# Kernel tuning notes

Measured on AMD Instinct MI355X. Metric: run time of the kernel, lower is better.

Reference implementation:

```python
import jax, jax.numpy as jnp
import numpy as np

# ---- problem constants (match init_kwargs) ----
LAM = 1.0; MU = 1.0; D0 = 1.0; NMIN = 1.0; NMAX = 99; ALPHA = 2.0
BATCH = 2048; N_STEPS = 64; T = 1.0; HIDDEN = 128


def _U(x):
    return D0 / (x + NMIN) ** ALPHA


def _delta_n(pre_n, dt, forward, k, rng):
    # faithful numpy port of PolymerDiffusion.delta_N (jump sizes shared across batch per call)
    log_res = -np.log(rng.random(k))
    lsk = np.concatenate([[0.0], np.cumsum(log_res / LAM / 2)])
    msk = np.concatenate([[0.0], np.cumsum(log_res / MU / 2)])
    jl = int(np.searchsorted(lsk[1:], dt, side='right'))  # first j with dt < lsk[j+1]
    jm = int(np.searchsorted(msk[1:], dt, side='right'))
    if jl >= k: jl = 0  # no break -> delta stays 0
    if jm >= k: jm = 0
    eta = rng.random(pre_n.shape[0])
    if forward:
        d_up = np.where(pre_n <= NMAX - jl, jl, 0)
        d_dn = np.where(pre_n >= jm, -jm, 0)
    else:
        d_up = np.where(pre_n >= jl, jl, 0)
        d_dn = np.where(pre_n <= NMAX - jm, -jm, 0)
    return np.where(eta < 0.5, d_up, d_dn).astype(np.float64)


def _get_samples(dt, N, rng):
    B = BATCH
    X1 = np.zeros((B, N + 1)); X1[:, 0] = rng.integers(0, NMAX + 1, B)
    X2 = np.zeros((B, N + 1))
    dB = rng.standard_normal((B, N)) * np.sqrt(dt)
    for i in range(N):
        X1[:, i + 1] = X1[:, i] + _delta_n(X1[:, i], dt, True, 5, rng)
        X2[:, i + 1] = X2[:, i] + _U(X1[:, i]) * dt + dB[:, i]
    X1b = rng.integers(0, NMAX + 1, (B, N + 1)).astype(np.float64)
    X2b = np.zeros((B, N + 1))
    dBb = rng.standard_normal((B, N)) * np.sqrt(dt)
    X1b[:, N] = X1[:, N]; X2b[:, N] = X2[:, N]
    for i in range(N):
        X1b[:, N - i - 1] = X1b[:, N - i] - _delta_n(X1b[:, N - i], dt, False, 5, rng)
        X2b[:, N - i - 1] = X2b[:, N - i] - _U(X1b[:, N - i]) * dt - dBb[:, N - i - 1]
    return (np.concatenate([X1, X1b], 0), np.concatenate([X2, X2b], 0), np.concatenate([dB, dBb], 0))


def setup_inputs() -> dict:
    rng = np.random.default_rng(0)
    dt = T / N_STEPS
    n_np, s_np, dB_np = _get_samples(dt, N_STEPS, rng)
    key = jax.random.key(0)
    ks = jax.random.split(key, 4)
    def w(k, fi, fo):
        return jax.random.normal(k, (fi, fo), jnp.float32) / np.sqrt(fi).astype(np.float32)
    return {
        'W1': w(ks[0], 2, HIDDEN), 'b1': jnp.zeros(HIDDEN, jnp.float32),
        'W2': w(ks[1], HIDDEN, HIDDEN), 'b2': jnp.zeros(HIDDEN, jnp.float32),
        'W3': w(ks[2], HIDDEN, HIDDEN), 'b3': jnp.zeros(HIDDEN, jnp.float32),
        'W4': w(ks[3], HIDDEN, NMAX + 1), 'b4': jnp.zeros(NMAX + 1, jnp.float32),
        'samples_n': jnp.asarray(n_np, jnp.int32),      # [2B, N+1]
        'samples_s': jnp.asarray(s_np, jnp.float32),    # [2B, N+1]
        'samples_deltaB': jnp.asarray(dB_np, jnp.float32),  # [2B, N]
        't': jnp.float32(T),
    }


def reference(W1, b1, W2, b2, W3, b3, W4, b4, samples_n, samples_s, samples_deltaB, t):
    N = samples_deltaB.shape[1]
    dt = t / N
    out_dim = W4.shape[1]  # nmax + 1

    def u_scalar(s, tk, n):
        x = jnp.stack([s, tk])  # [2]
        h = jnp.tanh(x @ W1 + b1)
        h = jnp.tanh(h @ W2 + b2)
        h = jnp.tanh(h @ W3 + b3)
        return (h @ W4 + b4)[n]

    du = jax.grad(u_scalar, 0)
    ddu = jax.grad(du, 0)
    u_v = jax.vmap(u_scalar)
    du_v = jax.vmap(du)
    ddu_v = jax.vmap(ddu)

    B2 = samples_s.shape[0]
    tk0 = jnp.broadcast_to(t, (B2,))
    sN, nN = samples_s[:, N], samples_n[:, N]
    u = u_v(sN, tk0, nN)
    ps = du_v(sN, tk0, nN)
    pss = ddu_v(sN, tk0, nN)

    # step i uses column N-1-i and time tk = t - i*dt (tk decremented AFTER get_partial, as in source)
    dB_rev = samples_deltaB[:, ::-1].T            # [N, 2B]
    s_rev = samples_s[:, N - 1::-1].T             # [N, 2B]
    n_rev = samples_n[:, N - 1::-1].T             # [N, 2B]
    tks = t - dt * jnp.arange(N, dtype=samples_s.dtype)  # [N]

    def step(carry, xs):
        u, ps, pss = carry
        dB, s_col, n_col, tk = xs
        u = u - ps * dB - pss * dt * 0.5
        tkv = jnp.broadcast_to(tk, s_col.shape)
        ps = du_v(s_col, tkv, n_col)
        pss = ddu_v(s_col, tkv, n_col)
        return (u, ps, pss), None

    (u, _, _), _ = jax.lax.scan(step, (u, ps, pss), (dB_rev, s_rev, n_rev, tks))

    beta = 1e6
    s0 = samples_s[:, 0]
    u0 = jnp.sqrt(beta / (2 * jnp.pi)) * jnp.exp(-beta * s0 ** 2 / 2) / out_dim
    return (u[:, None], u0[:, None])
```

## Files before the change

kernel.cpp:

```cpp
#include <hip/hip_runtime.h>
#include <hip/hip_fp16.h>
#include <math.h>

#define HIDDEN 128
#define NSTEP  64
#define BATCH2 4096
#define OUTD   100

typedef __attribute__((ext_vector_type(4))) _Float16 f16x4;
typedef __attribute__((ext_vector_type(8))) _Float16 f16x8;
typedef __attribute__((ext_vector_type(4))) float    f32x4;

static __device__ __forceinline__ f32x4 mfma16(f16x4 a, f16x4 b, f32x4 c) {
    return __builtin_amdgcn_mfma_f32_16x16x16f16(a, b, c, 0, 0, 0);
}
static __device__ __forceinline__ unsigned h2u(__half2 h) {
    return __builtin_bit_cast(unsigned, h);
}
static __device__ __forceinline__ __half2 u2h(unsigned u) {
    return __builtin_bit_cast(__half2, u);
}
static __device__ __forceinline__ f16x4 frag2(__half2 lo, __half2 hi) {
    uint2 p = { h2u(lo), h2u(hi) };
    return __builtin_bit_cast(f16x4, p);
}

static __device__ __forceinline__ void load_lds16(const void* g, void* l) {
    __builtin_amdgcn_global_load_lds(
        (const __attribute__((address_space(1))) void*)g,
        (__attribute__((address_space(3))) void*)l, 16, 0, 0);
}

static __device__ __forceinline__ void tanh_chain_h2(
    __half2 z, __half2 zd, __half2 zdd,
    __half2& a, __half2& ad, __half2& add)
{
    const __half2 one = __float2half2_rn(1.0f);
    const __half2 two = __float2half2_rn(2.0f);
    __half2 e = h2exp(__hadd2(z, z));
    __half2 w = __hmul2(two, h2rcp(__hadd2(e, one)));
    a  = __hsub2(one, w);
    __half2 g = __hmul2(w, __hsub2(two, w));
    ad = __hmul2(g, zd);
    __half2 p = __hmul2(a, zd);
    __half2 u = __hadd2(p, p);
    add = __hsub2(__hmul2(g, zdd), __hmul2(u, ad));
}

__global__ __launch_bounds__(256) void setup_kernel(
    const float* __restrict__ W2, const float* __restrict__ W3,
    const float* __restrict__ W4,
    const float* __restrict__ samples_s,
    __half* __restrict__ wbf, float* __restrict__ out)
{
    int t = blockIdx.x * blockDim.x + threadIdx.x;
    int l   = t >> 14;
    int pos = t & 16383;
    int chunk = pos >> 9;
    int mt = chunk >> 2, kp = chunk & 3;
    int lane = (pos >> 3) & 63;
    int i = pos & 7;
    int row = 16 * mt + (lane & 15);
    int k   = 32 * kp + 16 * (i >> 2) + 4 * (lane >> 4) + (i & 3);
    const float* W = l ? W3 : W2;
    wbf[t] = __float2half(W[k * HIDDEN + row]);
    if (t < OUTD * HIDDEN) {
        int nn = t >> 7, h = t & 127;
        wbf[32768 + t] = __float2half(W4[h * OUTD + nn]);
    }
    if (t < BATCH2) {
        out[t] = 0.0f;
        float s0 = samples_s[t * (NSTEP + 1)];
        out[BATCH2 + t] = 3.9894228040143267f * expf(-500000.0f * s0 * s0);
    }
}

__global__ __launch_bounds__(256, 3) void eval_kernel(
    const float* __restrict__ W1, const float* __restrict__ b1,
    const float* __restrict__ b2, const float* __restrict__ b3,
    const float* __restrict__ b4,
    const __half* __restrict__ wbf,
    const int*   __restrict__ samples_n,
    const float* __restrict__ samples_s,
    const float* __restrict__ samples_dB,
    const float* __restrict__ tptr,
    float* __restrict__ out)
{
    __shared__ __align__(16) short ldsW[HIDDEN * HIDDEN];
    __shared__ float ldsB2[HIDDEN];
    __shared__ float ldsB3[HIDDEN];

    const int tid  = threadIdx.x;
    const int w    = tid >> 6;
    const int lane = tid & 63;
    const int m16  = lane & 15;
    const int q    = lane >> 4;
    const int b    = blockIdx.x;

    if (tid < HIDDEN) {
        ldsB2[tid] = b2[tid];
        ldsB3[tid] = b3[tid];
    }
    {
        const short* g2 = (const short*)wbf;
        #pragma unroll
        for (int it = 0; it < 8; ++it) {
            int idx = w * 8 + it;
            load_lds16(g2 + idx * 512 + lane * 8, ldsW + idx * 512);
        }
    }

    const float t  = tptr[0];
    const float dt = t / (float)NSTEP;
    const int   j  = 16 * w + m16;
    const int   c  = NSTEP - j;
    const float s  = samples_s[b * (NSTEP + 1) + c];
    const int   n  = samples_n[b * (NSTEP + 1) + c];
    const float dB = samples_dB[b * NSTEP + (NSTEP - 1 - j)];
    const float tk = (j == 0) ? t : t - dt * (float)(j - 1);

    f16x4 Bv[8], Bd[8], Bdd[8];
    const __half2 zero2 = __float2half2_rn(0.0f);
    #pragma unroll
    for (int kt = 0; kt < 8; ++kt) {
        const int h0 = 16 * kt + 4 * q;
        float4 wa = *(const float4*)(W1 + h0);
        float4 wb = *(const float4*)(W1 + HIDDEN + h0);
        float4 bb = *(const float4*)(b1 + h0);
        __half2 z0 = __floats2half2_rn(fmaf(wa.x, s, fmaf(wb.x, tk, bb.x)),
                                       fmaf(wa.y, s, fmaf(wb.y, tk, bb.y)));
        __half2 z1 = __floats2half2_rn(fmaf(wa.z, s, fmaf(wb.z, tk, bb.z)),
                                       fmaf(wa.w, s, fmaf(wb.w, tk, bb.w)));
        __half2 zd0 = __floats2half2_rn(wa.x, wa.y);
        __half2 zd1 = __floats2half2_rn(wa.z, wa.w);
        __half2 a0, ad0, add0, a1, ad1, add1;
        tanh_chain_h2(z0, zd0, zero2, a0, ad0, add0);
        tanh_chain_h2(z1, zd1, zero2, a1, ad1, add1);
        Bv[kt]  = frag2(a0,  a1);
        Bd[kt]  = frag2(ad0, ad1);
        Bdd[kt] = frag2(add0, add1);
    }

    __syncthreads();

    f16x4 Nv[8], Nd[8], Ndd[8];
    #pragma unroll
    for (int mt = 0; mt < 8; ++mt) {
        f32x4 aV = {0.f,0.f,0.f,0.f}, aD = {0.f,0.f,0.f,0.f}, aDD = {0.f,0.f,0.f,0.f};
        #pragma unroll
        for (int kp = 0; kp < 4; ++kp) {
            f16x8 aw = *(const f16x8*)(ldsW + ((mt * 4 + kp) << 9) + (lane << 3));
            f16x4 alo = (f16x4){aw[0], aw[1], aw[2], aw[3]};
            f16x4 ahi = (f16x4){aw[4], aw[5], aw[6], aw[7]};
            aV  = mfma16(alo, Bv [2*kp], aV );
            aD  = mfma16(alo, Bd [2*kp], aD );
            aDD = mfma16(alo, Bdd[2*kp], aDD);
            aV  = mfma16(ahi, Bv [2*kp+1], aV );
            aD  = mfma16(ahi, Bd [2*kp+1], aD );
            aDD = mfma16(ahi, Bdd[2*kp+1], aDD);
        }
        const int h0 = 16 * mt + 4 * q;
        float4 bias = *(const float4*)(ldsB2 + h0);
        __half2 a0, ad0, add0, a1, ad1, add1;
        tanh_chain_h2(__floats2half2_rn(aV[0] + bias.x, aV[1] + bias.y),
                      __floats2half2_rn(aD[0], aD[1]),
                      __floats2half2_rn(aDD[0], aDD[1]), a0, ad0, add0);
        tanh_chain_h2(__floats2half2_rn(aV[2] + bias.z, aV[3] + bias.w),
                      __floats2half2_rn(aD[2], aD[3]),
                      __floats2half2_rn(aDD[2], aDD[3]), a1, ad1, add1);
        Nv[mt]  = frag2(a0,  a1);
        Nd[mt]  = frag2(ad0, ad1);
        Ndd[mt] = frag2(add0, add1);
    }

    __syncthreads();

    {
        const short* g3 = (const short*)(wbf + HIDDEN * HIDDEN);
        #pragma unroll
        for (int it = 0; it < 8; ++it) {
            int idx = w * 8 + it;
            load_lds16(g3 + idx * 512 + lane * 8, ldsW + idx * 512);
        }
    }
    __syncthreads();

    const __half* __restrict__ w4t = wbf + 2 * HIDDEN * HIDDEN;
    __half2 accV = zero2, accD = zero2, accDD = zero2;
    #pragma unroll
    for (int mt = 0; mt < 8; ++mt) {
        f32x4 aV = {0.f,0.f,0.f,0.f}, aD = {0.f,0.f,0.f,0.f}, aDD = {0.f,0.f,0.f,0.f};
        #pragma unroll
        for (int kp = 0; kp < 4; ++kp) {
            f16x8 aw = *(const f16x8*)(ldsW + ((mt * 4 + kp) << 9) + (lane << 3));
            f16x4 alo = (f16x4){aw[0], aw[1], aw[2], aw[3]};
            f16x4 ahi = (f16x4){aw[4], aw[5], aw[6], aw[7]};
            aV  = mfma16(alo, Nv [2*kp], aV );
            aD  = mfma16(alo, Nd [2*kp], aD );
            aDD = mfma16(alo, Ndd[2*kp], aDD);
            aV  = mfma16(ahi, Nv [2*kp+1], aV );
            aD  = mfma16(ahi, Nd [2*kp+1], aD );
            aDD = mfma16(ahi, Ndd[2*kp+1], aDD);
        }
        const int h0 = 16 * mt + 4 * q;
        float4 bias = *(const float4*)(ldsB3 + h0);
        uint2 w4u = *(const uint2*)(w4t + n * HIDDEN + h0);
        __half2 w4lo = u2h(w4u.x), w4hi = u2h(w4u.y);
        __half2 a0, ad0, add0, a1, ad1, add1;
        tanh_chain_h2(__floats2half2_rn(aV[0] + bias.x, aV[1] + bias.y),
                      __floats2half2_rn(aD[0], aD[1]),
                      __floats2half2_rn(aDD[0], aDD[1]), a0, ad0, add0);
        tanh_chain_h2(__floats2half2_rn(aV[2] + bias.z, aV[3] + bias.w),
                      __floats2half2_rn(aD[2], aD[3]),
                      __floats2half2_rn(aDD[2], aDD[3]), a1, ad1, add1);
        accV  = __hfma2(a0,  w4lo, accV );  accV  = __hfma2(a1,  w4hi, accV );
        accD  = __hfma2(ad0, w4lo, accD );  accD  = __hfma2(ad1, w4hi, accD );
        accDD = __hfma2(add0, w4lo, accDD); accDD = __hfma2(add1, w4hi, accDD);
    }
    float sv  = __low2float(accV)  + __high2float(accV);
    float sd  = __low2float(accD)  + __high2float(accD);
    float sdd = __low2float(accDD) + __high2float(accDD);

    sd  += __shfl_xor(sd,  16, 64);  sd  += __shfl_xor(sd,  32, 64);
    sdd += __shfl_xor(sdd, 16, 64);  sdd += __shfl_xor(sdd, 32, 64);
    sv  += __shfl_xor(sv,  16, 64);  sv  += __shfl_xor(sv,  32, 64);

    float contrib = -(sd * dB + sdd * dt * 0.5f);
    if (j == 0) contrib += sv + b4[n];

    contrib += __shfl_xor(contrib, 1, 64);
    contrib += __shfl_xor(contrib, 2, 64);
    contrib += __shfl_xor(contrib, 4, 64);
    contrib += __shfl_xor(contrib, 8, 64);
    if (lane == 0) atomicAdd(&out[b], contrib);
}

extern "C" void kernel_launch(void* const* d_in, const int* in_sizes, int n_in,
                              void* d_out, int out_size, void* d_ws, size_t ws_size,
                              hipStream_t stream) {
    const float* W1 = (const float*)d_in[0];
    const float* b1 = (const float*)d_in[1];
    const float* W2 = (const float*)d_in[2];
    const float* b2 = (const float*)d_in[3];
    const float* W3 = (const float*)d_in[4];
    const float* b3 = (const float*)d_in[5];
    const float* W4 = (const float*)d_in[6];
    const float* b4 = (const float*)d_in[7];
    const int*   sn  = (const int*)d_in[8];
    const float* ss  = (const float*)d_in[9];
    const float* sdB = (const float*)d_in[10];
    const float* t   = (const float*)d_in[11];
    float* out = (float*)d_out;
    __half* wbf = (__half*)d_ws;

    setup_kernel<<<(2 * HIDDEN * HIDDEN) / 256, 256, 0, stream>>>(W2, W3, W4, ss, wbf, out);
    eval_kernel<<<BATCH2, 256, 0, stream>>>(
        W1, b1, b2, b3, b4, wbf, sn, ss, sdB, t, out);
}
```

Baseline: 160.4 us.

## Switch to 16x16x32 f16 MFMA with repacked weights and bias-initialized accumulators

Replaces the pairs of 16x16x16 f16 MFMAs with single 16x16x32 MFMAs (available on gfx950), which means repacking the W2 layout in the setup kernel and reshaping the layer-1 and layer-2 activation fragments into 8-wide K chunks. The layer-2 output fragments are concatenated so they serve directly as B operands for the layer-3 MFMA. Biases now seed the accumulators straight from global memory instead of being staged in LDS and added afterwards, and the occupancy hint is raised from 3 to 5 blocks per CU. This halves the MFMA instruction count and drops the bias LDS traffic, at the cost of possible register pressure under the tighter launch bound.

```diff
diff --git a/kernel.cpp b/kernel.cpp
--- a/kernel.cpp
+++ b/kernel.cpp
@@ -7,12 +7,11 @@
 #define BATCH2 4096
 #define OUTD   100
 
-typedef __attribute__((ext_vector_type(4))) _Float16 f16x4;
 typedef __attribute__((ext_vector_type(8))) _Float16 f16x8;
 typedef __attribute__((ext_vector_type(4))) float    f32x4;
 
-static __device__ __forceinline__ f32x4 mfma16(f16x4 a, f16x4 b, f32x4 c) {
-    return __builtin_amdgcn_mfma_f32_16x16x16f16(a, b, c, 0, 0, 0);
+static __device__ __forceinline__ f32x4 mfma32(f16x8 a, f16x8 b, f32x4 c) {
+    return __builtin_amdgcn_mfma_f32_16x16x32_f16(a, b, c, 0, 0, 0);
 }
 static __device__ __forceinline__ unsigned h2u(__half2 h) {
     return __builtin_bit_cast(unsigned, h);
@@ -20,9 +19,13 @@
 static __device__ __forceinline__ __half2 u2h(unsigned u) {
     return __builtin_bit_cast(__half2, u);
 }
-static __device__ __forceinline__ f16x4 frag2(__half2 lo, __half2 hi) {
-    uint2 p = { h2u(lo), h2u(hi) };
-    return __builtin_bit_cast(f16x4, p);
+static __device__ __forceinline__ f16x8 frag8(__half2 a, __half2 b, __half2 c, __half2 d) {
+    uint4 p = { h2u(a), h2u(b), h2u(c), h2u(d) };
+    return __builtin_bit_cast(f16x8, p);
+}
+static __device__ __forceinline__ f16x8 catu2(uint2 lo, uint2 hi) {
+    uint4 p = { lo.x, lo.y, hi.x, hi.y };
+    return __builtin_bit_cast(f16x8, p);
 }
 
 static __device__ __forceinline__ void load_lds16(const void* g, void* l) {
@@ -56,14 +59,20 @@
     int t = blockIdx.x * blockDim.x + threadIdx.x;
     int l   = t >> 14;
     int pos = t & 16383;
-    int chunk = pos >> 9;
-    int mt = chunk >> 2, kp = chunk & 3;
+    int c    = (pos >> 9) & 3;
     int lane = (pos >> 3) & 63;
-    int i = pos & 7;
-    int row = 16 * mt + (lane & 15);
-    int k   = 32 * kp + 16 * (i >> 2) + 4 * (lane >> 4) + (i & 3);
-    const float* W = l ? W3 : W2;
-    wbf[t] = __float2half(W[k * HIDDEN + row]);
+    int i    = pos & 7;
+    int m    = ((pos >> 11) << 4) + (lane & 15);
+    int q    = lane >> 4;
+    float v;
+    if (l == 0) {
+        int k = 32 * c + 8 * q + i;
+        v = W2[k * HIDDEN + m];
+    } else {
+        int lg = 32 * c + 16 * (i >> 2) + 4 * q + (i & 3);
+        v = W3[lg * HIDDEN + m];
+    }
+    wbf[t] = __float2half(v);
     if (t < OUTD * HIDDEN) {
         int nn = t >> 7, h = t & 127;
         wbf[32768 + t] = __float2half(W4[h * OUTD + nn]);
@@ -75,7 +84,7 @@
     }
 }
 
-__global__ __launch_bounds__(256, 3) void eval_kernel(
+__global__ __launch_bounds__(256, 5) void eval_kernel(
     const float* __restrict__ W1, const float* __restrict__ b1,
     const float* __restrict__ b2, const float* __restrict__ b3,
     const float* __restrict__ b4,
@@ -87,8 +96,6 @@
     float* __restrict__ out)
 {
     __shared__ __align__(16) short ldsW[HIDDEN * HIDDEN];
-    __shared__ float ldsB2[HIDDEN];
-    __shared__ float ldsB3[HIDDEN];
 
     const int tid  = threadIdx.x;
     const int w    = tid >> 6;
@@ -97,10 +104,6 @@
     const int q    = lane >> 4;
     const int b    = blockIdx.x;
 
-    if (tid < HIDDEN) {
-        ldsB2[tid] = b2[tid];
-        ldsB3[tid] = b3[tid];
-    }
     {
         const short* g2 = (const short*)wbf;
         #pragma unroll
@@ -119,58 +122,63 @@
     const float dB = samples_dB[b * NSTEP + (NSTEP - 1 - j)];
     const float tk = (j == 0) ? t : t - dt * (float)(j - 1);
 
-    f16x4 Bv[8], Bd[8], Bdd[8];
+    f16x8 B1v[4], B1d[4], B1dd[4];
     const __half2 zero2 = __float2half2_rn(0.0f);
     #pragma unroll
-    for (int kt = 0; kt < 8; ++kt) {
-        const int h0 = 16 * kt + 4 * q;
-        float4 wa = *(const float4*)(W1 + h0);
-        float4 wb = *(const float4*)(W1 + HIDDEN + h0);
-        float4 bb = *(const float4*)(b1 + h0);
-        __half2 z0 = __floats2half2_rn(fmaf(wa.x, s, fmaf(wb.x, tk, bb.x)),
-                                       fmaf(wa.y, s, fmaf(wb.y, tk, bb.y)));
-        __half2 z1 = __floats2half2_rn(fmaf(wa.z, s, fmaf(wb.z, tk, bb.z)),
-                                       fmaf(wa.w, s, fmaf(wb.w, tk, bb.w)));
-        __half2 zd0 = __floats2half2_rn(wa.x, wa.y);
-        __half2 zd1 = __floats2half2_rn(wa.z, wa.w);
+    for (int ck = 0; ck < 4; ++ck) {
+        const int h0 = 32 * ck + 8 * q;
+        float4 wa0 = *(const float4*)(W1 + h0);
+        float4 wa1 = *(const float4*)(W1 + h0 + 4);
+        float4 wb0 = *(const float4*)(W1 + HIDDEN + h0);
+        float4 wb1 = *(const float4*)(W1 + HIDDEN + h0 + 4);
+        float4 bb0 = *(const float4*)(b1 + h0);
+        float4 bb1 = *(const float4*)(b1 + h0 + 4);
+        __half2 a[4], ad[4], add[4];
+        {
+            __half2 z  = __floats2half2_rn(fmaf(wa0.x, s, fmaf(wb0.x, tk, bb0.x)),
+                                           fmaf(wa0.y, s, fmaf(wb0.y, tk, bb0.y)));
+            tanh_chain_h2(z, __floats2half2_rn(wa0.x, wa0.y), zero2, a[0], ad[0], add[0]);
+            z  = __floats2half2_rn(fmaf(wa0.z, s, fmaf(wb0.z, tk, bb0.z)),
+                                   fmaf(wa0.w, s, fmaf(wb0.w, tk, bb0.w)));
+            tanh_chain_h2(z, __floats2half2_rn(wa0.z, wa0.w), zero2, a[1], ad[1], add[1]);
+            z  = __floats2half2_rn(fmaf(wa1.x, s, fmaf(wb1.x, tk, bb1.x)),
+                                   fmaf(wa1.y, s, fmaf(wb1.y, tk, bb1.y)));
+            tanh_chain_h2(z, __floats2half2_rn(wa1.x, wa1.y), zero2, a[2], ad[2], add[2]);
+            z  = __floats2half2_rn(fmaf(wa1.z, s, fmaf(wb1.z, tk, bb1.z)),
+                                   fmaf(wa1.w, s, fmaf(wb1.w, tk, bb1.w)));
+            tanh_chain_h2(z, __floats2half2_rn(wa1.z, wa1.w), zero2, a[3], ad[3], add[3]);
+        }
+        B1v[ck]  = frag8(a[0],  a[1],  a[2],  a[3]);
+        B1d[ck]  = frag8(ad[0], ad[1], ad[2], ad[3]);
+        B1dd[ck] = frag8(add[0], add[1], add[2], add[3]);
+    }
+
+    __syncthreads();
+
+    uint2 Nv[8], Nd[8], Ndd[8];
+    #pragma unroll
+    for (int mt = 0; mt < 8; ++mt) {
+        const int h0 = 16 * mt + 4 * q;
+        float4 bias = *(const float4*)(b2 + h0);
+        f32x4 aV = {bias.x, bias.y, bias.z, bias.w};
+        f32x4 aD = {0.f,0.f,0.f,0.f}, aDD = {0.f,0.f,0.f,0.f};
+        #pragma unroll
+        for (int ck = 0; ck < 4; ++ck) {
+            f16x8 aw = *(const f16x8*)(ldsW + ((mt * 4 + ck) << 9) + (lane << 3));
+            aV  = mfma32(aw, B1v[ck],  aV );
+            aD  = mfma32(aw, B1d[ck],  aD );
+            aDD = mfma32(aw, B1dd[ck], aDD);
+        }
         __half2 a0, ad0, add0, a1, ad1, add1;
-        tanh_chain_h2(z0, zd0, zero2, a0, ad0, add0);
-        tanh_chain_h2(z1, zd1, zero2, a1, ad1, add1);
-        Bv[kt]  = frag2(a0,  a1);
-        Bd[kt]  = frag2(ad0, ad1);
-        Bdd[kt] = frag2(add0, add1);
-    }
-
-    __syncthreads();
-
-    f16x4 Nv[8], Nd[8], Ndd[8];
-    #pragma unroll
-    for (int mt = 0; mt < 8; ++mt) {
-        f32x4 aV = {0.f,0.f,0.f,0.f}, aD = {0.f,0.f,0.f,0.f}, aDD = {0.f,0.f,0.f,0.f};
-        #pragma unroll
-        for (int kp = 0; kp < 4; ++kp) {
-            f16x8 aw = *(const f16x8*)(ldsW + ((mt * 4 + kp) << 9) + (lane << 3));
-            f16x4 alo = (f16x4){aw[0], aw[1], aw[2], aw[3]};
-            f16x4 ahi = (f16x4){aw[4], aw[5], aw[6], aw[7]};
-            aV  = mfma16(alo, Bv [2*kp], aV );
-            aD  = mfma16(alo, Bd [2*kp], aD );
-            aDD = mfma16(alo, Bdd[2*kp], aDD);
-            aV  = mfma16(ahi, Bv [2*kp+1], aV );
-            aD  = mfma16(ahi, Bd [2*kp+1], aD );
-            aDD = mfma16(ahi, Bdd[2*kp+1], aDD);
-        }
-        const int h0 = 16 * mt + 4 * q;
-        float4 bias = *(const float4*)(ldsB2 + h0);
-        __half2 a0, ad0, add0, a1, ad1, add1;
-        tanh_chain_h2(__floats2half2_rn(aV[0] + bias.x, aV[1] + bias.y),
+        tanh_chain_h2(__floats2half2_rn(aV[0], aV[1]),
                       __floats2half2_rn(aD[0], aD[1]),
                       __floats2half2_rn(aDD[0], aDD[1]), a0, ad0, add0);
-        tanh_chain_h2(__floats2half2_rn(aV[2] + bias.z, aV[3] + bias.w),
+        tanh_chain_h2(__floats2half2_rn(aV[2], aV[3]),
                       __floats2half2_rn(aD[2], aD[3]),
                       __floats2half2_rn(aDD[2], aDD[3]), a1, ad1, add1);
-        Nv[mt]  = frag2(a0,  a1);
-        Nd[mt]  = frag2(ad0, ad1);
-        Ndd[mt] = frag2(add0, add1);
+        Nv[mt]  = (uint2){ h2u(a0),  h2u(a1)  };
+        Nd[mt]  = (uint2){ h2u(ad0), h2u(ad1) };
+        Ndd[mt] = (uint2){ h2u(add0), h2u(add1) };
     }
 
     __syncthreads();
@@ -183,34 +191,38 @@
             load_lds16(g3 + idx * 512 + lane * 8, ldsW + idx * 512);
         }
     }
+
+    f16x8 B2v[4], B2d[4], B2dd[4];
+    #pragma unroll
+    for (int ck = 0; ck < 4; ++ck) {
+        B2v[ck]  = catu2(Nv[2*ck],  Nv[2*ck+1]);
+        B2d[ck]  = catu2(Nd[2*ck],  Nd[2*ck+1]);
+        B2dd[ck] = catu2(Ndd[2*ck], Ndd[2*ck+1]);
+    }
     __syncthreads();
 
     const __half* __restrict__ w4t = wbf + 2 * HIDDEN * HIDDEN;
     __half2 accV = zero2, accD = zero2, accDD = zero2;
     #pragma unroll
     for (int mt = 0; mt < 8; ++mt) {
-        f32x4 aV = {0.f,0.f,0.f,0.f}, aD = {0.f,0.f,0.f,0.f}, aDD = {0.f,0.f,0.f,0.f};
-        #pragma unroll
-        for (int kp = 0; kp < 4; ++kp) {
-            f16x8 aw = *(const f16x8*)(ldsW + ((mt * 4 + kp) << 9) + (lane << 3));
-            f16x4 alo = (f16x4){aw[0], aw[1], aw[2], aw[3]};
-            f16x4 ahi = (f16x4){aw[4], aw[5], aw[6], aw[7]};
-            aV  = mfma16(alo, Nv [2*kp], aV );
-            aD  = mfma16(alo, Nd [2*kp], aD );
-            aDD = mfma16(alo, Ndd[2*kp], aDD);
-            aV  = mfma16(ahi, Nv [2*kp+1], aV );
-            aD  = mfma16(ahi, Nd [2*kp+1], aD );
-            aDD = mfma16(ahi, Ndd[2*kp+1], aDD);
-        }
         const int h0 = 16 * mt + 4 * q;
-        float4 bias = *(const float4*)(ldsB3 + h0);
+        float4 bias = *(const float4*)(b3 + h0);
+        f32x4 aV = {bias.x, bias.y, bias.z, bias.w};
+        f32x4 aD = {0.f,0.f,0.f,0.f}, aDD = {0.f,0.f,0.f,0.f};
+        #pragma unroll
+        for (int ck = 0; ck < 4; ++ck) {
+            f16x8 aw = *(const f16x8*)(ldsW + ((mt * 4 + ck) << 9) + (lane << 3));
+            aV  = mfma32(aw, B2v[ck],  aV );
+            aD  = mfma32(aw, B2d[ck],  aD );
+            aDD = mfma32(aw, B2dd[ck], aDD);
+        }
         uint2 w4u = *(const uint2*)(w4t + n * HIDDEN + h0);
         __half2 w4lo = u2h(w4u.x), w4hi = u2h(w4u.y);
         __half2 a0, ad0, add0, a1, ad1, add1;
-        tanh_chain_h2(__floats2half2_rn(aV[0] + bias.x, aV[1] + bias.y),
+        tanh_chain_h2(__floats2half2_rn(aV[0], aV[1]),
                       __floats2half2_rn(aD[0], aD[1]),
                       __floats2half2_rn(aDD[0], aDD[1]), a0, ad0, add0);
-        tanh_chain_h2(__floats2half2_rn(aV[2] + bias.z, aV[3] + bias.w),
+        tanh_chain_h2(__floats2half2_rn(aV[2], aV[3]),
                       __floats2half2_rn(aD[2], aD[3]),
                       __floats2half2_rn(aDD[2], aDD[3]), a1, ad1, add1);
         accV  = __hfma2(a0,  w4lo, accV );  accV  = __hfma2(a1,  w4hi, accV );
```

Measured after the change: 164.8 us. 2.7% more time.
